# Performance work log

Hardware: AMD Instinct MI355X
Metric: run time of the kernel (lower is better)

Reference implementation:

```python
import jax, jax.numpy as jnp
import numpy as np

NUM_HEADS = 16
WIN_H, WIN_W = 7, 7
DIM = 512
N = WIN_H * WIN_W  # 49 tokens per window
B_ = 2048          # num_windows * batch
NUM_WINDOWS = 64


def _relative_pos_indices(win_h, win_w):
    ch, cw = np.meshgrid(np.arange(win_h), np.arange(win_w), indexing='ij')
    coords = np.stack([ch, cw], axis=-1).reshape(-1, 2)          # (N, 2)
    rel = coords[None, :, :] - coords[:, None, :]                # (N, N, 2)
    rel[:, :, 0] += win_h - 1
    rel[:, :, 1] += win_w - 1
    rel[:, :, 0] *= 2 * win_w - 1
    return rel.sum(-1).reshape(-1).astype(np.int32)             # (N*N,)


def setup_inputs() -> dict:
    key = jax.random.key(0)
    k1, k2, k3, k4, k5 = jax.random.split(key, 5)
    x = jax.random.normal(k1, (B_, N, DIM), dtype=jnp.float32)
    # 0 / -100 shift mask (finite stand-in for -inf; same softmax effect)
    u = jax.random.uniform(k2, (NUM_WINDOWS, N, N))
    mask = jnp.where(u < 0.2, -100.0, 0.0).astype(jnp.float32)
    qkv_w = jax.random.normal(k3, (DIM, 3 * DIM), dtype=jnp.float32) * 0.02
    qkv_b = jnp.zeros((3 * DIM,), jnp.float32)
    proj_w = jax.random.normal(k4, (DIM, DIM), dtype=jnp.float32) * 0.02
    proj_b = jnp.zeros((DIM,), jnp.float32)
    bias_table = jax.random.normal(k5, ((2 * WIN_H - 1) * (2 * WIN_W - 1), NUM_HEADS), dtype=jnp.float32) * 0.02
    rel_idx = jnp.asarray(_relative_pos_indices(WIN_H, WIN_W))
    return {"x": x, "mask": mask, "qkv_w": qkv_w, "qkv_b": qkv_b,
            "proj_w": proj_w, "proj_b": proj_b,
            "bias_table": bias_table, "rel_idx": rel_idx}


def reference(x, mask, qkv_w, qkv_b, proj_w, proj_b, bias_table, rel_idx):
    b_, n, c = x.shape
    h = NUM_HEADS
    d = c // h
    scale = d ** -0.5
    qkv = (x @ qkv_w + qkv_b).reshape(b_, n, 3, h, d)
    q, k, v = jnp.moveaxis(qkv, 2, 0)                 # each (b_, n, h, d)
    attn = jnp.einsum('bnhd,bmhd->bhnm', q * scale, k)  # (b_, h, n, n)
    # relative-position bias gather: (n*n,) -> (n, n, h) -> (h, n, n)
    bias = bias_table[rel_idx].reshape(n, n, h).transpose(2, 0, 1)
    attn = attn + bias[None]
    nw = mask.shape[0]
    attn = attn.reshape(b_ // nw, nw, h, n, n) + mask[None, :, None]
    attn = jax.nn.softmax(attn.reshape(b_, h, n, n), axis=-1)
    out = jnp.einsum('bhnm,bmhd->bnhd', attn, v).reshape(b_, n, c)
    return out @ proj_w + proj_b
```

## Files before the change

### kernel.cpp

```cpp
#include <hip/hip_runtime.h>
#include <stdint.h>

typedef __attribute__((ext_vector_type(8))) short short8;
typedef __attribute__((ext_vector_type(8))) unsigned short ushort8;
typedef __attribute__((ext_vector_type(4))) float float4_t;

#define AS1 __attribute__((address_space(1)))
#define AS3 __attribute__((address_space(3)))

__device__ __forceinline__ unsigned short f2bf(float f) {
    union { float f; unsigned u; } c; c.f = f;
    return (unsigned short)((c.u + 0x7fffu + ((c.u >> 16) & 1u)) >> 16);
}

__device__ __forceinline__ void load16_lds(const void* g, void* l) {
    __builtin_amdgcn_global_load_lds((const AS1 void*)(uintptr_t)g,
                                     (AS3 void*)(uintptr_t)l, 16, 0, 0);
}

__global__ __launch_bounds__(256)
void cvt_x(const float4_t* __restrict__ x, unsigned short* __restrict__ xb, int n8) {
    int i = blockIdx.x * 256 + threadIdx.x;
    if (i >= n8) return;
    float4_t a = x[2 * i], b = x[2 * i + 1];
    ushort8 v;
    v[0] = f2bf(a[0]); v[1] = f2bf(a[1]); v[2] = f2bf(a[2]); v[3] = f2bf(a[3]);
    v[4] = f2bf(b[0]); v[5] = f2bf(b[1]); v[6] = f2bf(b[2]); v[7] = f2bf(b[3]);
    ((ushort8*)xb)[i] = v;
}

__global__ __launch_bounds__(256)
void prep(const float* __restrict__ qkv_w, const float* __restrict__ proj_w,
          const float* __restrict__ bias_tab, const int* __restrict__ rel_idx,
          unsigned short* __restrict__ qkv_wT, unsigned short* __restrict__ proj_wT,
          float* __restrict__ biasD) {
    int i = blockIdx.x * 256 + threadIdx.x;
    if (i < 786432) {
        int n = i >> 9, k = i & 511;
        qkv_wT[i] = f2bf(qkv_w[k * 1536 + n]);
    } else if (i < 1048576) {
        int j = i - 786432;
        int n = j >> 9, k = j & 511;
        proj_wT[j] = f2bf(proj_w[k * 512 + n]);
    } else if (i < 1086992) {
        int j = i - 1048576;
        int h = j / 2401, mn = j % 2401;
        biasD[j] = bias_tab[rel_idx[mn] * 16 + h];
    }
}

template <int MODE>
__global__ __launch_bounds__(256)
void gemm_bt(const unsigned short* __restrict__ A, const unsigned short* __restrict__ B,
             void* __restrict__ Cv, const float* __restrict__ bias,
             int M, int N, int K, float qscale) {
    __shared__ __align__(16) unsigned short As[128 * 32];
    __shared__ __align__(16) unsigned short Bs[128 * 32];

    const int t = threadIdx.x;
    const int lane = t & 63;
    const int wave = t >> 6;
    const int col = lane & 15;
    const int quad = lane >> 4;
    const int wm = (wave & 1) * 64;
    const int wn = (wave >> 1) * 64;
    const int m0 = blockIdx.y * 128;
    const int n0 = blockIdx.x * 128;

    float4_t acc[4][4] = {};

    const int row = t >> 2;
    const int seg = t & 3;
    const unsigned short* Ag0 = A + (size_t)(m0 + row) * K + seg * 8;
    const unsigned short* Ag1 = A + (size_t)(m0 + 64 + row) * K + seg * 8;
    const unsigned short* Bg0 = B + (size_t)(n0 + row) * K + seg * 8;
    const unsigned short* Bg1 = B + (size_t)(n0 + 64 + row) * K + seg * 8;

    for (int kk = 0; kk < K; kk += 32) {
        __syncthreads();
        load16_lds(Ag0 + kk, &As[t * 8]);
        load16_lds(Ag1 + kk, &As[2048 + t * 8]);
        load16_lds(Bg0 + kk, &Bs[t * 8]);
        load16_lds(Bg1 + kk, &Bs[2048 + t * 8]);
        __syncthreads();

        short8 a[4], b[4];
#pragma unroll
        for (int i = 0; i < 4; ++i)
            a[i] = *(const short8*)&As[(wm + i * 16 + col) * 32 + quad * 8];
#pragma unroll
        for (int j = 0; j < 4; ++j)
            b[j] = *(const short8*)&Bs[(wn + j * 16 + col) * 32 + quad * 8];
#pragma unroll
        for (int i = 0; i < 4; ++i)
#pragma unroll
            for (int j = 0; j < 4; ++j)
                acc[i][j] = __builtin_amdgcn_mfma_f32_16x16x32_bf16(a[i], b[j], acc[i][j], 0, 0, 0);
    }

    if (MODE == 0) {
        unsigned short* C = (unsigned short*)Cv;
#pragma unroll
        for (int j = 0; j < 4; ++j) {
            int gc = n0 + wn + j * 16 + col;
            float bv = bias[gc];
            float sc = (gc < 512) ? qscale : 1.0f;
#pragma unroll
            for (int i = 0; i < 4; ++i)
#pragma unroll
                for (int r = 0; r < 4; ++r) {
                    int gr = m0 + wm + i * 16 + quad * 4 + r;
                    C[(size_t)gr * N + gc] = f2bf((acc[i][j][r] + bv) * sc);
                }
        }
    } else {
        float* C = (float*)Cv;
#pragma unroll
        for (int j = 0; j < 4; ++j) {
            int gc = n0 + wn + j * 16 + col;
            float bv = bias[gc];
#pragma unroll
            for (int i = 0; i < 4; ++i)
#pragma unroll
                for (int r = 0; r < 4; ++r) {
                    int gr = m0 + wm + i * 16 + quad * 4 + r;
                    C[(size_t)gr * N + gc] = acc[i][j][r] + bv;
                }
        }
    }
}

__global__ __launch_bounds__(64)
void attn_win(const unsigned short* __restrict__ qkv,
              const float* __restrict__ mask,
              const float* __restrict__ biasD,
              unsigned short* __restrict__ attn_out) {
    __shared__ __align__(16) unsigned short P[64 * 64];
    __shared__ __align__(16) unsigned short Vt[32 * 64];

    const int bh = blockIdx.x;
    const int w = bh >> 4;
    const int hh = bh & 15;
    const int lane = threadIdx.x;
    const int col = lane & 15;
    const int quad = lane >> 4;
    const size_t rowbase = (size_t)(w * 49) * 1536;

    {
        ushort8 u0 = {}, u1 = {}, u2 = {}, u3 = {};
        if (lane < 49) {
            const ushort8* vp = (const ushort8*)(qkv + rowbase + (size_t)lane * 1536 + 1024 + hh * 32);
            u0 = vp[0]; u1 = vp[1]; u2 = vp[2]; u3 = vp[3];
        }
#pragma unroll
        for (int c = 0; c < 8; ++c) {
            Vt[(c) * 64 + lane] = u0[c];
            Vt[(c + 8) * 64 + lane] = u1[c];
            Vt[(c + 16) * 64 + lane] = u2[c];
            Vt[(c + 24) * 64 + lane] = u3[c];
        }
    }

    float4_t s[4][4] = {};
    {
        short8 qf[4], kf[4];
#pragma unroll
        for (int i = 0; i < 4; ++i) {
            int m = i * 16 + col; if (m > 48) m = 48;
            qf[i] = *(const short8*)(qkv + rowbase + (size_t)m * 1536 + hh * 32 + quad * 8);
            int n = i * 16 + col; if (n > 48) n = 48;
            kf[i] = *(const short8*)(qkv + rowbase + (size_t)n * 1536 + 512 + hh * 32 + quad * 8);
        }
#pragma unroll
        for (int i = 0; i < 4; ++i)
#pragma unroll
            for (int j = 0; j < 4; ++j)
                s[i][j] = __builtin_amdgcn_mfma_f32_16x16x32_bf16(qf[i], kf[j], s[i][j], 0, 0, 0);
    }

    const float* mk = mask + (size_t)(w & 63) * 2401;
    const float* bs = biasD + (size_t)hh * 2401;
#pragma unroll
    for (int j = 0; j < 4; ++j) {
        int n = j * 16 + col;
#pragma unroll
        for (int i = 0; i < 4; ++i)
#pragma unroll
            for (int r = 0; r < 4; ++r) {
                int m = i * 16 + quad * 4 + r;
                float v = s[i][j][r];
                if (n < 49) { if (m < 49) v += mk[m * 49 + n] + bs[m * 49 + n]; }
                else v = -1e30f;
                s[i][j][r] = v;
            }
    }

#pragma unroll
    for (int i = 0; i < 4; ++i)
#pragma unroll
        for (int r = 0; r < 4; ++r) {
            float mx = fmaxf(fmaxf(s[i][0][r], s[i][1][r]), fmaxf(s[i][2][r], s[i][3][r]));
#pragma unroll
            for (int off = 1; off < 16; off <<= 1)
                mx = fmaxf(mx, __shfl_xor(mx, off, 16));
            float e0 = __expf(s[i][0][r] - mx);
            float e1 = __expf(s[i][1][r] - mx);
            float e2 = __expf(s[i][2][r] - mx);
            float e3 = __expf(s[i][3][r] - mx);
            float sum = e0 + e1 + e2 + e3;
#pragma unroll
            for (int off = 1; off < 16; off <<= 1)
                sum += __shfl_xor(sum, off, 16);
            float inv = 1.0f / sum;
            s[i][0][r] = e0 * inv; s[i][1][r] = e1 * inv;
            s[i][2][r] = e2 * inv; s[i][3][r] = e3 * inv;
        }

#pragma unroll
    for (int i = 0; i < 4; ++i)
#pragma unroll
        for (int r = 0; r < 4; ++r) {
            int m = i * 16 + quad * 4 + r;
#pragma unroll
            for (int j = 0; j < 4; ++j)
                P[m * 64 + j * 16 + col] = f2bf(s[i][j][r]);
        }
    __syncthreads();

    float4_t o[4][2] = {};
#pragma unroll
    for (int s2 = 0; s2 < 2; ++s2) {
        short8 pa[4], vb[2];
#pragma unroll
        for (int i = 0; i < 4; ++i)
            pa[i] = *(const short8*)&P[(i * 16 + col) * 64 + s2 * 32 + quad * 8];
#pragma unroll
        for (int tj = 0; tj < 2; ++tj)
            vb[tj] = *(const short8*)&Vt[(tj * 16 + col) * 64 + s2 * 32 + quad * 8];
#pragma unroll
        for (int i = 0; i < 4; ++i)
#pragma unroll
            for (int tj = 0; tj < 2; ++tj)
                o[i][tj] = __builtin_amdgcn_mfma_f32_16x16x32_bf16(pa[i], vb[tj], o[i][tj], 0, 0, 0);
    }

#pragma unroll
    for (int i = 0; i < 4; ++i)
#pragma unroll
        for (int r = 0; r < 4; ++r) {
            int m = i * 16 + quad * 4 + r;
            if (m < 49) {
                size_t ob = (size_t)(w * 49 + m) * 512 + hh * 32;
                attn_out[ob + col] = f2bf(o[i][0][r]);
                attn_out[ob + 16 + col] = f2bf(o[i][1][r]);
            }
        }
}

extern "C" void kernel_launch(void* const* d_in, const int* in_sizes, int n_in,
                              void* d_out, int out_size, void* d_ws, size_t ws_size,
                              hipStream_t stream) {
    const float* x        = (const float*)d_in[0];
    const float* mask     = (const float*)d_in[1];
    const float* qkv_w    = (const float*)d_in[2];
    const float* qkv_b    = (const float*)d_in[3];
    const float* proj_w   = (const float*)d_in[4];
    const float* proj_b   = (const float*)d_in[5];
    const float* bias_tab = (const float*)d_in[6];
    const int*   rel_idx  = (const int*)d_in[7];
    float* out = (float*)d_out;

    char* ws = (char*)d_ws;
    size_t off = 0;
    auto carve = [&](size_t bytes) -> char* {
        char* p = ws + off;
        off += (bytes + 255) & ~(size_t)255;
        return p;
    };
    unsigned short* x_bf    = (unsigned short*)carve((size_t)51380224 * 2);
    unsigned short* qkv_wT  = (unsigned short*)carve((size_t)786432 * 2);
    unsigned short* proj_wT = (unsigned short*)carve((size_t)262144 * 2);
    float*          biasD   = (float*)carve((size_t)38416 * 4);
    unsigned short* qkv_o   = (unsigned short*)carve((size_t)100352 * 1536 * 2);
    unsigned short* attn_o  = x_bf;

    cvt_x<<<25088, 256, 0, stream>>>((const float4_t*)x, x_bf, 6422528);
    prep<<<4247, 256, 0, stream>>>(qkv_w, proj_w, bias_tab, rel_idx, qkv_wT, proj_wT, biasD);
    gemm_bt<0><<<dim3(12, 784), 256, 0, stream>>>(x_bf, qkv_wT, (void*)qkv_o, qkv_b,
                                                  100352, 1536, 512, 0.17677669529663687f);
    attn_win<<<32768, 64, 0, stream>>>(qkv_o, mask, biasD, attn_o);
    gemm_bt<1><<<dim3(4, 784), 256, 0, stream>>>(attn_o, proj_wT, (void*)out, proj_b,
                                                 100352, 512, 512, 1.0f);
}
```

Baseline: 971.7 us.

## Double-buffer GEMM LDS, swizzle blocks for XCDs, vectorize epilogues and pad mask/bias

The GEMM kernel gains double-buffered LDS loads that prefetch the next K tile while computing the current one. It also gets a 1D grid remapped across the 8 XCDs, and swapped MFMA operands so each lane holds 4 contiguous columns, which allows vector stores. The attention kernel now reads mask and bias from tables padded to 64 columns, so masking needs no bounds checks. It also uses an XOR-swizzled LDS layout to avoid bank conflicts, a row-wise softmax needing only two shuffles, and vectorized bf16 stores. This adds larger prep work and more LDS use in the GEMM, which may reduce occupancy.

```diff
diff --git a/kernel.cpp b/kernel.cpp
--- a/kernel.cpp
+++ b/kernel.cpp
@@ -3,6 +3,7 @@
 
 typedef __attribute__((ext_vector_type(8))) short short8;
 typedef __attribute__((ext_vector_type(8))) unsigned short ushort8;
+typedef __attribute__((ext_vector_type(4))) unsigned short bf16x4;
 typedef __attribute__((ext_vector_type(4))) float float4_t;
 
 #define AS1 __attribute__((address_space(1)))
@@ -16,6 +17,12 @@
 __device__ __forceinline__ void load16_lds(const void* g, void* l) {
     __builtin_amdgcn_global_load_lds((const AS1 void*)(uintptr_t)g,
                                      (AS3 void*)(uintptr_t)l, 16, 0, 0);
+}
+
+__device__ __forceinline__ void wait_vm0_barrier() {
+    asm volatile("s_waitcnt vmcnt(0)" ::: "memory");
+    __builtin_amdgcn_s_barrier();
+    asm volatile("" ::: "memory");
 }
 
 __global__ __launch_bounds__(256)
@@ -32,8 +39,9 @@
 __global__ __launch_bounds__(256)
 void prep(const float* __restrict__ qkv_w, const float* __restrict__ proj_w,
           const float* __restrict__ bias_tab, const int* __restrict__ rel_idx,
+          const float* __restrict__ mask,
           unsigned short* __restrict__ qkv_wT, unsigned short* __restrict__ proj_wT,
-          float* __restrict__ biasD) {
+          float* __restrict__ biasP, float* __restrict__ maskP) {
     int i = blockIdx.x * 256 + threadIdx.x;
     if (i < 786432) {
         int n = i >> 9, k = i & 511;
@@ -42,10 +50,16 @@
         int j = i - 786432;
         int n = j >> 9, k = j & 511;
         proj_wT[j] = f2bf(proj_w[k * 512 + n]);
-    } else if (i < 1086992) {
+    } else if (i < 1098752) {
         int j = i - 1048576;
-        int h = j / 2401, mn = j % 2401;
-        biasD[j] = bias_tab[rel_idx[mn] * 16 + h];
+        int h = j / 3136, mn = j % 3136;
+        int m = mn >> 6, n = mn & 63;
+        biasP[j] = (n < 49) ? bias_tab[rel_idx[m * 49 + n] * 16 + h] : 0.0f;
+    } else {
+        int j = i - 1098752;
+        int w = j / 3136, mn = j % 3136;
+        int m = mn >> 6, n = mn & 63;
+        maskP[j] = (n < 49) ? mask[w * 2401 + m * 49 + n] : -1e30f;
     }
 }
 
@@ -54,8 +68,8 @@
 void gemm_bt(const unsigned short* __restrict__ A, const unsigned short* __restrict__ B,
              void* __restrict__ Cv, const float* __restrict__ bias,
              int M, int N, int K, float qscale) {
-    __shared__ __align__(16) unsigned short As[128 * 32];
-    __shared__ __align__(16) unsigned short Bs[128 * 32];
+    __shared__ __align__(16) unsigned short As[2][128 * 32];
+    __shared__ __align__(16) unsigned short Bs[2][128 * 32];
 
     const int t = threadIdx.x;
     const int lane = t & 63;
@@ -64,8 +78,13 @@
     const int quad = lane >> 4;
     const int wm = (wave & 1) * 64;
     const int wn = (wave >> 1) * 64;
-    const int m0 = blockIdx.y * 128;
-    const int n0 = blockIdx.x * 128;
+
+    const int nwg = gridDim.x;
+    const int cpx = nwg >> 3;
+    const int wg = (blockIdx.x & 7) * cpx + (blockIdx.x >> 3);
+    const int nbx = N >> 7;
+    const int m0 = (wg / nbx) * 128;
+    const int n0 = (wg % nbx) * 128;
 
     float4_t acc[4][4] = {};
 
@@ -76,64 +95,74 @@
     const unsigned short* Bg0 = B + (size_t)(n0 + row) * K + seg * 8;
     const unsigned short* Bg1 = B + (size_t)(n0 + 64 + row) * K + seg * 8;
 
+    load16_lds(Ag0, &As[0][t * 8]);
+    load16_lds(Ag1, &As[0][2048 + t * 8]);
+    load16_lds(Bg0, &Bs[0][t * 8]);
+    load16_lds(Bg1, &Bs[0][2048 + t * 8]);
+    wait_vm0_barrier();
+
+    int cur = 0;
     for (int kk = 0; kk < K; kk += 32) {
-        __syncthreads();
-        load16_lds(Ag0 + kk, &As[t * 8]);
-        load16_lds(Ag1 + kk, &As[2048 + t * 8]);
-        load16_lds(Bg0 + kk, &Bs[t * 8]);
-        load16_lds(Bg1 + kk, &Bs[2048 + t * 8]);
-        __syncthreads();
-
+        if (kk + 32 < K) {
+            int nb = cur ^ 1;
+            load16_lds(Ag0 + kk + 32, &As[nb][t * 8]);
+            load16_lds(Ag1 + kk + 32, &As[nb][2048 + t * 8]);
+            load16_lds(Bg0 + kk + 32, &Bs[nb][t * 8]);
+            load16_lds(Bg1 + kk + 32, &Bs[nb][2048 + t * 8]);
+        }
         short8 a[4], b[4];
 #pragma unroll
         for (int i = 0; i < 4; ++i)
-            a[i] = *(const short8*)&As[(wm + i * 16 + col) * 32 + quad * 8];
+            a[i] = *(const short8*)&As[cur][(wm + i * 16 + col) * 32 + quad * 8];
 #pragma unroll
         for (int j = 0; j < 4; ++j)
-            b[j] = *(const short8*)&Bs[(wn + j * 16 + col) * 32 + quad * 8];
+            b[j] = *(const short8*)&Bs[cur][(wn + j * 16 + col) * 32 + quad * 8];
 #pragma unroll
         for (int i = 0; i < 4; ++i)
 #pragma unroll
             for (int j = 0; j < 4; ++j)
-                acc[i][j] = __builtin_amdgcn_mfma_f32_16x16x32_bf16(a[i], b[j], acc[i][j], 0, 0, 0);
+                acc[i][j] = __builtin_amdgcn_mfma_f32_16x16x32_bf16(b[j], a[i], acc[i][j], 0, 0, 0);
+
+        wait_vm0_barrier();
+        cur ^= 1;
     }
 
     if (MODE == 0) {
         unsigned short* C = (unsigned short*)Cv;
 #pragma unroll
         for (int j = 0; j < 4; ++j) {
-            int gc = n0 + wn + j * 16 + col;
-            float bv = bias[gc];
-            float sc = (gc < 512) ? qscale : 1.0f;
-#pragma unroll
-            for (int i = 0; i < 4; ++i)
-#pragma unroll
-                for (int r = 0; r < 4; ++r) {
-                    int gr = m0 + wm + i * 16 + quad * 4 + r;
-                    C[(size_t)gr * N + gc] = f2bf((acc[i][j][r] + bv) * sc);
-                }
+            int gc0 = n0 + wn + j * 16 + quad * 4;
+            float4_t bv = *(const float4_t*)&bias[gc0];
+            float sc = (gc0 < 512) ? qscale : 1.0f;
+#pragma unroll
+            for (int i = 0; i < 4; ++i) {
+                int gr = m0 + wm + i * 16 + col;
+                bf16x4 u;
+#pragma unroll
+                for (int r = 0; r < 4; ++r) u[r] = f2bf((acc[i][j][r] + bv[r]) * sc);
+                *(bf16x4*)&C[(size_t)gr * N + gc0] = u;
+            }
         }
     } else {
         float* C = (float*)Cv;
 #pragma unroll
         for (int j = 0; j < 4; ++j) {
-            int gc = n0 + wn + j * 16 + col;
-            float bv = bias[gc];
-#pragma unroll
-            for (int i = 0; i < 4; ++i)
-#pragma unroll
-                for (int r = 0; r < 4; ++r) {
-                    int gr = m0 + wm + i * 16 + quad * 4 + r;
-                    C[(size_t)gr * N + gc] = acc[i][j][r] + bv;
-                }
+            int gc0 = n0 + wn + j * 16 + quad * 4;
+            float4_t bv = *(const float4_t*)&bias[gc0];
+#pragma unroll
+            for (int i = 0; i < 4; ++i) {
+                int gr = m0 + wm + i * 16 + col;
+                float4_t ov = acc[i][j] + bv;
+                *(float4_t*)&C[(size_t)gr * N + gc0] = ov;
+            }
         }
     }
 }
 
 __global__ __launch_bounds__(64)
 void attn_win(const unsigned short* __restrict__ qkv,
-              const float* __restrict__ mask,
-              const float* __restrict__ biasD,
+              const float* __restrict__ maskP,
+              const float* __restrict__ biasP,
               unsigned short* __restrict__ attn_out) {
     __shared__ __align__(16) unsigned short P[64 * 64];
     __shared__ __align__(16) unsigned short Vt[32 * 64];
@@ -154,10 +183,10 @@
         }
 #pragma unroll
         for (int c = 0; c < 8; ++c) {
-            Vt[(c) * 64 + lane] = u0[c];
-            Vt[(c + 8) * 64 + lane] = u1[c];
-            Vt[(c + 16) * 64 + lane] = u2[c];
-            Vt[(c + 24) * 64 + lane] = u3[c];
+            Vt[((c) * 64 + lane) ^ ((c & 7) << 3)] = u0[c];
+            Vt[((c + 8) * 64 + lane) ^ ((c & 7) << 3)] = u1[c];
+            Vt[((c + 16) * 64 + lane) ^ ((c & 7) << 3)] = u2[c];
+            Vt[((c + 24) * 64 + lane) ^ ((c & 7) << 3)] = u3[c];
         }
     }
 
@@ -168,63 +197,61 @@
         for (int i = 0; i < 4; ++i) {
             int m = i * 16 + col; if (m > 48) m = 48;
             qf[i] = *(const short8*)(qkv + rowbase + (size_t)m * 1536 + hh * 32 + quad * 8);
-            int n = i * 16 + col; if (n > 48) n = 48;
-            kf[i] = *(const short8*)(qkv + rowbase + (size_t)n * 1536 + 512 + hh * 32 + quad * 8);
+            kf[i] = *(const short8*)(qkv + rowbase + (size_t)m * 1536 + 512 + hh * 32 + quad * 8);
         }
 #pragma unroll
         for (int i = 0; i < 4; ++i)
 #pragma unroll
             for (int j = 0; j < 4; ++j)
-                s[i][j] = __builtin_amdgcn_mfma_f32_16x16x32_bf16(qf[i], kf[j], s[i][j], 0, 0, 0);
-    }
-
-    const float* mk = mask + (size_t)(w & 63) * 2401;
-    const float* bs = biasD + (size_t)hh * 2401;
-#pragma unroll
-    for (int j = 0; j < 4; ++j) {
-        int n = j * 16 + col;
-#pragma unroll
-        for (int i = 0; i < 4; ++i)
+                s[i][j] = __builtin_amdgcn_mfma_f32_16x16x32_bf16(kf[j], qf[i], s[i][j], 0, 0, 0);
+    }
+
+    {
+        const float* mk = maskP + (size_t)(w & 63) * 3136;
+        const float* bs = biasP + (size_t)hh * 3136;
+#pragma unroll
+        for (int i = 0; i < 4; ++i) {
+            int mc = i * 16 + col; if (mc > 48) mc = 48;
+#pragma unroll
+            for (int j = 0; j < 4; ++j) {
+                int n0 = j * 16 + quad * 4;
+                float4_t a4 = *(const float4_t*)&mk[mc * 64 + n0];
+                float4_t b4 = *(const float4_t*)&bs[mc * 64 + n0];
+#pragma unroll
+                for (int r = 0; r < 4; ++r) s[i][j][r] += a4[r] + b4[r];
+            }
+        }
+    }
+
+#pragma unroll
+    for (int i = 0; i < 4; ++i) {
+        int m = i * 16 + col;
+        float mx = s[i][0][0];
+#pragma unroll
+        for (int j = 0; j < 4; ++j)
+#pragma unroll
+            for (int r = 0; r < 4; ++r) mx = fmaxf(mx, s[i][j][r]);
+        mx = fmaxf(mx, __shfl_xor(mx, 16));
+        mx = fmaxf(mx, __shfl_xor(mx, 32));
+        float sum = 0.f;
+#pragma unroll
+        for (int j = 0; j < 4; ++j)
 #pragma unroll
             for (int r = 0; r < 4; ++r) {
-                int m = i * 16 + quad * 4 + r;
-                float v = s[i][j][r];
-                if (n < 49) { if (m < 49) v += mk[m * 49 + n] + bs[m * 49 + n]; }
-                else v = -1e30f;
-                s[i][j][r] = v;
-            }
-    }
-
-#pragma unroll
-    for (int i = 0; i < 4; ++i)
-#pragma unroll
-        for (int r = 0; r < 4; ++r) {
-            float mx = fmaxf(fmaxf(s[i][0][r], s[i][1][r]), fmaxf(s[i][2][r], s[i][3][r]));
-#pragma unroll
-            for (int off = 1; off < 16; off <<= 1)
-                mx = fmaxf(mx, __shfl_xor(mx, off, 16));
-            float e0 = __expf(s[i][0][r] - mx);
-            float e1 = __expf(s[i][1][r] - mx);
-            float e2 = __expf(s[i][2][r] - mx);
-            float e3 = __expf(s[i][3][r] - mx);
-            float sum = e0 + e1 + e2 + e3;
-#pragma unroll
-            for (int off = 1; off < 16; off <<= 1)
-                sum += __shfl_xor(sum, off, 16);
-            float inv = 1.0f / sum;
-            s[i][0][r] = e0 * inv; s[i][1][r] = e1 * inv;
-            s[i][2][r] = e2 * inv; s[i][3][r] = e3 * inv;
-        }
-
-#pragma unroll
-    for (int i = 0; i < 4; ++i)
-#pragma unroll
-        for (int r = 0; r < 4; ++r) {
-            int m = i * 16 + quad * 4 + r;
-#pragma unroll
-            for (int j = 0; j < 4; ++j)
-                P[m * 64 + j * 16 + col] = f2bf(s[i][j][r]);
-        }
+                float e = __expf(s[i][j][r] - mx);
+                s[i][j][r] = e; sum += e;
+            }
+        sum += __shfl_xor(sum, 16);
+        sum += __shfl_xor(sum, 32);
+        float inv = 1.0f / sum;
+#pragma unroll
+        for (int j = 0; j < 4; ++j) {
+            bf16x4 u;
+#pragma unroll
+            for (int r = 0; r < 4; ++r) u[r] = f2bf(s[i][j][r] * inv);
+            *(bf16x4*)&P[(m * 64 + j * 16 + quad * 4) ^ ((m & 7) << 3)] = u;
+        }
+    }
     __syncthreads();
 
     float4_t o[4][2] = {};
@@ -232,29 +259,36 @@
     for (int s2 = 0; s2 < 2; ++s2) {
         short8 pa[4], vb[2];
 #pragma unroll
+        for (int i = 0; i < 4; ++i) {
+            int m = i * 16 + col;
+            pa[i] = *(const short8*)&P[(m * 64 + s2 * 32 + quad * 8) ^ ((m & 7) << 3)];
+        }
+#pragma unroll
+        for (int tj = 0; tj < 2; ++tj) {
+            int d = tj * 16 + col;
+            vb[tj] = *(const short8*)&Vt[(d * 64 + s2 * 32 + quad * 8) ^ ((d & 7) << 3)];
+        }
+#pragma unroll
         for (int i = 0; i < 4; ++i)
-            pa[i] = *(const short8*)&P[(i * 16 + col) * 64 + s2 * 32 + quad * 8];
-#pragma unroll
-        for (int tj = 0; tj < 2; ++tj)
-            vb[tj] = *(const short8*)&Vt[(tj * 16 + col) * 64 + s2 * 32 + quad * 8];
-#pragma unroll
-        for (int i = 0; i < 4; ++i)
 #pragma unroll
             for (int tj = 0; tj < 2; ++tj)
-                o[i][tj] = __builtin_amdgcn_mfma_f32_16x16x32_bf16(pa[i], vb[tj], o[i][tj], 0, 0, 0);
-    }
-
-#pragma unroll
-    for (int i = 0; i < 4; ++i)
-#pragma unroll
-        for (int r = 0; r < 4; ++r) {
-            int m = i * 16 + quad * 4 + r;
-            if (m < 49) {
-                size_t ob = (size_t)(w * 49 + m) * 512 + hh * 32;
-                attn_out[ob + col] = f2bf(o[i][0][r]);
-                attn_out[ob + 16 + col] = f2bf(o[i][1][r]);
-            }
-        }
+                o[i][tj] = __builtin_amdgcn_mfma_f32_16x16x32_bf16(vb[tj], pa[i], o[i][tj], 0, 0, 0);
+    }
+
+#pragma unroll
+    for (int i = 0; i < 4; ++i) {
+        int m = i * 16 + col;
+        if (m < 49) {
+            size_t ob = (size_t)(w * 49 + m) * 512 + hh * 32 + quad * 4;
+#pragma unroll
+            for (int tj = 0; tj < 2; ++tj) {
+                bf16x4 u;
+#pragma unroll
+                for (int r = 0; r < 4; ++r) u[r] = f2bf(o[i][tj][r]);
+                *(bf16x4*)&attn_out[ob + tj * 16] = u;
+            }
+        }
+    }
 }
 
 extern "C" void kernel_launch(void* const* d_in, const int* in_sizes, int n_in,
@@ -280,15 +314,17 @@
     unsigned short* x_bf    = (unsigned short*)carve((size_t)51380224 * 2);
     unsigned short* qkv_wT  = (unsigned short*)carve((size_t)786432 * 2);
     unsigned short* proj_wT = (unsigned short*)carve((size_t)262144 * 2);
-    float*          biasD   = (float*)carve((size_t)38416 * 4);
+    float*          biasP   = (float*)carve((size_t)50176 * 4);
+    float*          maskP   = (float*)carve((size_t)200704 * 4);
     unsigned short* qkv_o   = (unsigned short*)carve((size_t)100352 * 1536 * 2);
     unsigned short* attn_o  = x_bf;
 
     cvt_x<<<25088, 256, 0, stream>>>((const float4_t*)x, x_bf, 6422528);
-    prep<<<4247, 256, 0, stream>>>(qkv_w, proj_w, bias_tab, rel_idx, qkv_wT, proj_wT, biasD);
-    gemm_bt<0><<<dim3(12, 784), 256, 0, stream>>>(x_bf, qkv_wT, (void*)qkv_o, qkv_b,
-                                                  100352, 1536, 512, 0.17677669529663687f);
-    attn_win<<<32768, 64, 0, stream>>>(qkv_o, mask, biasD, attn_o);
-    gemm_bt<1><<<dim3(4, 784), 256, 0, stream>>>(attn_o, proj_wT, (void*)out, proj_b,
-                                                 100352, 512, 512, 1.0f);
-}
+    prep<<<5076, 256, 0, stream>>>(qkv_w, proj_w, bias_tab, rel_idx, mask,
+                                   qkv_wT, proj_wT, biasP, maskP);
+    gemm_bt<0><<<9408, 256, 0, stream>>>(x_bf, qkv_wT, (void*)qkv_o, qkv_b,
+                                         100352, 1536, 512, 0.17677669529663687f);
+    attn_win<<<32768, 64, 0, stream>>>(qkv_o, maskP, biasP, attn_o);
+    gemm_bt<1><<<3136, 256, 0, stream>>>(attn_o, proj_wT, (void*)out, proj_b,
+                                         100352, 512, 512, 1.0f);
+}
```

Result: faster. 934.5 us (-3.8%).
